# Performance work log

Hardware: AMD Instinct MI355X
Metric: run time of the kernel (lower is better)

Reference implementation:

```python
import jax, jax.numpy as jnp
import numpy as np

WH, WW = 8, 8
NUM_HEADS = 8
DIM = 256
MLP_HIDDEN = 1024
EPS = 1e-5


def _rel_pos_index(wh, ww):
    ch, cw = np.meshgrid(np.arange(wh), np.arange(ww), indexing='ij')
    flat = np.stack([ch.ravel(), cw.ravel()])            # (2, N)
    rel = flat[:, :, None] - flat[:, None, :]            # (2, N, N)
    rel = rel.transpose(1, 2, 0).copy()                  # (N, N, 2)
    rel[:, :, 0] += wh - 1
    rel[:, :, 1] += ww - 1
    rel[:, :, 0] *= 2 * ww - 1
    return jnp.asarray(rel.sum(-1))                      # (N, N) int

REL_IDX = _rel_pos_index(WH, WW)


def _layernorm(x, g, b):
    mu = x.mean(-1, keepdims=True)
    var = ((x - mu) ** 2).mean(-1, keepdims=True)
    return (x - mu) * jax.lax.rsqrt(var + EPS) * g + b


def _window_partition(x):
    B, H, W, C = x.shape
    x = x.reshape(B, H // WH, WH, W // WW, WW, C)
    return x.transpose(0, 1, 3, 2, 4, 5).reshape(-1, WH * WW, C)


def _window_reverse(w, B, H, W):
    C = w.shape[-1]
    x = w.reshape(B, H // WH, W // WW, WH, WW, C)
    return x.transpose(0, 1, 3, 2, 4, 5).reshape(B, H, W, C)


def _window_attn(qx, kvx, qw, qb, kvw, kvb, bias_table, pw, pb):
    # qx/kvx: [Bw, N, C]; weights stored as [in, out] (torch Linear transposed)
    Bw, N, C = qx.shape
    hd = C // NUM_HEADS
    scale = hd ** -0.5
    q = (qx @ qw + qb).reshape(Bw, N, NUM_HEADS, hd).transpose(0, 2, 1, 3) * scale
    kv = (kvx @ kvw + kvb).reshape(Bw, N, 2, NUM_HEADS, hd)
    k = kv[:, :, 0].transpose(0, 2, 1, 3)
    v = kv[:, :, 1].transpose(0, 2, 1, 3)
    attn = jnp.einsum('bhnd,bhmd->bhnm', q, k)
    bias = bias_table[REL_IDX.reshape(-1)].reshape(N, N, NUM_HEADS).transpose(2, 0, 1)
    attn = jax.nn.softmax(attn + bias[None], axis=-1)
    out = jnp.einsum('bhnm,bhmd->bhnd', attn, v).transpose(0, 2, 1, 3).reshape(Bw, N, C)
    return out @ pw + pb


def setup_inputs() -> dict:
    key = jax.random.key(0)
    ks = jax.random.split(key, 16)
    B, H, W, C = 4, 160, 160, DIM
    nW = (H // WH) * (W // WW)
    N = WH * WW
    n_bias = (2 * WH - 1) * (2 * WW - 1)  # 225
    s = 0.02
    return {
        'x': jax.random.normal(ks[0], (B, H, W, C), jnp.float32),
        'enc_feat': jax.random.normal(ks[1], (B, H, W, C), jnp.float32),
        'mask_matrix': jnp.zeros((nW, N, N), jnp.float32),
        'norm1_g': jnp.ones((C,), jnp.float32),
        'norm1_b': jnp.zeros((C,), jnp.float32),
        'q1_w': jax.random.normal(ks[2], (C, C), jnp.float32) * s,
        'q1_b': jnp.zeros((C,), jnp.float32),
        'kv1_w': jax.random.normal(ks[3], (C, 2 * C), jnp.float32) * s,
        'kv1_b': jnp.zeros((2 * C,), jnp.float32),
        'bias1': jax.random.normal(ks[4], (n_bias, NUM_HEADS), jnp.float32) * s,
        'proj1_w': jax.random.normal(ks[5], (C, C), jnp.float32) * s,
        'proj1_b': jnp.zeros((C,), jnp.float32),
        'q2_w': jax.random.normal(ks[6], (C, C), jnp.float32) * s,
        'q2_b': jnp.zeros((C,), jnp.float32),
        'kv2_w': jax.random.normal(ks[7], (C, 2 * C), jnp.float32) * s,
        'kv2_b': jnp.zeros((2 * C,), jnp.float32),
        'bias2': jax.random.normal(ks[8], (n_bias, NUM_HEADS), jnp.float32) * s,
        'proj2_w': jax.random.normal(ks[9], (C, C), jnp.float32) * s,
        'proj2_b': jnp.zeros((C,), jnp.float32),
        'norm2_g': jnp.ones((C,), jnp.float32),
        'norm2_b': jnp.zeros((C,), jnp.float32),
        'fc1_w': jax.random.normal(ks[10], (C, MLP_HIDDEN), jnp.float32) * s,
        'fc1_b': jnp.zeros((MLP_HIDDEN,), jnp.float32),
        'fc2_w': jax.random.normal(ks[11], (MLP_HIDDEN, C), jnp.float32) * s,
        'fc2_b': jnp.zeros((C,), jnp.float32),
    }


def reference(x, enc_feat, mask_matrix, norm1_g, norm1_b, q1_w, q1_b, kv1_w, kv1_b,
              bias1, proj1_w, proj1_b, q2_w, q2_b, kv2_w, kv2_b, bias2, proj2_w,
              proj2_b, norm2_g, norm2_b, fc1_w, fc1_b, fc2_w, fc2_b):
    # NOTE: the source forward never passes mask_matrix into attention; faithful here.
    B, H, W, C = x.shape
    shortcut = x
    xn = _layernorm(x, norm1_g, norm1_b)
    xw = _window_partition(xn)              # [B*nW, N, C]
    ew = _window_partition(enc_feat)        # [B*nW, N, C]
    # windowed self-attention with relative position bias
    xw = _window_attn(xw, xw, q1_w, q1_b, kv1_w, kv1_b, bias1, proj1_w, proj1_b)
    # windowed cross-attention to encoder features
    xw = _window_attn(xw, ew, q2_w, q2_b, kv2_w, kv2_b, bias2, proj2_w, proj2_b)
    x = shortcut + _window_reverse(xw, B, H, W)
    h = _layernorm(x, norm2_g, norm2_b)
    h = jax.nn.gelu(h @ fc1_w + fc1_b, approximate=False) @ fc2_w + fc2_b
    return x + h
```

## Files before the change

kernel.cpp:

```cpp
#include <hip/hip_runtime.h>

typedef __attribute__((ext_vector_type(4))) float f32x4;
typedef __attribute__((ext_vector_type(8))) short bf16x8;
typedef __attribute__((ext_vector_type(8))) unsigned short ushort8;
typedef unsigned short u16;
typedef unsigned int u32;

#define LDS_AS(p) ((__attribute__((address_space(3))) void*)(p))
#define GLB_AS(p) ((const __attribute__((address_space(1))) void*)(p))

__device__ __forceinline__ u16 f2b(float f) {
    u32 u = __builtin_bit_cast(u32, f);
    u32 r = (u + 0x7fffu + ((u >> 16) & 1u)) >> 16;
    return (u16)r;
}

struct PrepAll {
    const float* src[8];
    u16* dst[8];
    int K[8];
    int N[8];
};

__global__ __launch_bounds__(256) void prep_w(PrepAll p) {
    const int wi = blockIdx.y;
    const int K = p.K[wi], N = p.N[wi];
    const int e = blockIdx.x * 256 + threadIdx.x;
    if (e >= K * N) return;
    const int k = e / N, n = e % N;
    p.dst[wi][n * K + k] = f2b(p.src[wi][e]);
}

__global__ __launch_bounds__(64) void prep_bias(const float* __restrict__ t1,
                                                const float* __restrict__ t2,
                                                float* __restrict__ Bm) {
    const int j = threadIdx.x;
    const int i = blockIdx.x;
    const int hh = blockIdx.y;
    const int s = hh >> 3, h = hh & 7;
    const int idx = ((i >> 3) - (j >> 3) + 7) * 15 + ((i & 7) - (j & 7) + 7);
    const float* tab = s ? t2 : t1;
    Bm[(long)hh * 4096 + i * 64 + j] = tab[idx * 8 + h];
}

__global__ __launch_bounds__(256) void cast_bf(const float* __restrict__ in,
                                               u16* __restrict__ out) {
    const long i = (long)blockIdx.x * 256 + threadIdx.x;
    const float4 a = *(const float4*)(in + i * 8);
    const float4 b = *(const float4*)(in + i * 8 + 4);
    ushort8 o;
    o[0] = f2b(a.x); o[1] = f2b(a.y); o[2] = f2b(a.z); o[3] = f2b(a.w);
    o[4] = f2b(b.x); o[5] = f2b(b.y); o[6] = f2b(b.z); o[7] = f2b(b.w);
    *(ushort8*)(out + i * 8) = o;
}

__global__ __launch_bounds__(256) void ln256(const float* __restrict__ x,
                                             const float* __restrict__ g,
                                             const float* __restrict__ b,
                                             u16* __restrict__ out) {
    const int lane = threadIdx.x & 63;
    const long row = (long)blockIdx.x * 4 + (threadIdx.x >> 6);
    const float4 v = *(const float4*)(x + row * 256 + lane * 4);
    float s = v.x + v.y + v.z + v.w;
    float s2 = v.x * v.x + v.y * v.y + v.z * v.z + v.w * v.w;
#pragma unroll
    for (int off = 32; off > 0; off >>= 1) {
        s += __shfl_xor(s, off);
        s2 += __shfl_xor(s2, off);
    }
    const float mu = s * (1.f / 256.f);
    const float var = s2 * (1.f / 256.f) - mu * mu;
    const float rr = rsqrtf(var + 1e-5f);
    const int c = lane * 4;
    const float4 gv = *(const float4*)(g + c);
    const float4 bv = *(const float4*)(b + c);
    ushort4 o;
    o.x = f2b((v.x - mu) * rr * gv.x + bv.x);
    o.y = f2b((v.y - mu) * rr * gv.y + bv.y);
    o.z = f2b((v.z - mu) * rr * gv.z + bv.z);
    o.w = f2b((v.w - mu) * rr * gv.w + bv.w);
    *(ushort4*)(out + row * 256 + c) = o;
}

template <int EPI>
__global__ __launch_bounds__(256) void gemm128(const u16* __restrict__ A,
                                               const u16* __restrict__ Bt,
                                               const float* __restrict__ bias,
                                               const float* __restrict__ res,
                                               float scale, u16* outb, float* outf,
                                               int N, int K) {
    __shared__ u16 Alds[128 * 32];
    __shared__ u16 Blds[128 * 32];
    const int t = threadIdx.x;
    const int lane = t & 63;
    const int wave = t >> 6;
    const int wr = wave >> 1, wc = wave & 1;
    const int l15 = lane & 15, lg = lane >> 4;
    const long m0 = (long)blockIdx.x * 128;
    const int n0 = blockIdx.y * 128;

    const u16* Ag = A + (m0 + (t >> 2)) * K + (t & 3) * 8;
    const u16* Bg = Bt + (long)(n0 + (t >> 2)) * K + (t & 3) * 8;
    u16* Al = Alds + t * 8;
    u16* Bl = Blds + t * 8;

    f32x4 acc[4][4];
#pragma unroll
    for (int i = 0; i < 4; i++)
#pragma unroll
        for (int j = 0; j < 4; j++) acc[i][j] = (f32x4){0.f, 0.f, 0.f, 0.f};

    for (int k0 = 0; k0 < K; k0 += 32) {
        __syncthreads();
        __builtin_amdgcn_global_load_lds(GLB_AS(Ag + k0), LDS_AS(Al), 16, 0, 0);
        __builtin_amdgcn_global_load_lds(GLB_AS(Ag + (long)64 * K + k0), LDS_AS(Al + 2048), 16, 0, 0);
        __builtin_amdgcn_global_load_lds(GLB_AS(Bg + k0), LDS_AS(Bl), 16, 0, 0);
        __builtin_amdgcn_global_load_lds(GLB_AS(Bg + (long)64 * K + k0), LDS_AS(Bl + 2048), 16, 0, 0);
        __syncthreads();
        bf16x8 af[4], bfr[4];
#pragma unroll
        for (int i = 0; i < 4; i++)
            af[i] = *(const bf16x8*)(Alds + (wr * 64 + i * 16 + l15) * 32 + lg * 8);
#pragma unroll
        for (int i = 0; i < 4; i++)
            bfr[i] = *(const bf16x8*)(Blds + (wc * 64 + i * 16 + l15) * 32 + lg * 8);
#pragma unroll
        for (int mi = 0; mi < 4; mi++)
#pragma unroll
            for (int ni = 0; ni < 4; ni++)
                acc[mi][ni] = __builtin_amdgcn_mfma_f32_16x16x32_bf16(af[mi], bfr[ni], acc[mi][ni], 0, 0, 0);
    }

#pragma unroll
    for (int mi = 0; mi < 4; mi++) {
#pragma unroll
        for (int ni = 0; ni < 4; ni++) {
            const int col = n0 + wc * 64 + ni * 16 + l15;
            const float bv = bias[col];
#pragma unroll
            for (int r = 0; r < 4; r++) {
                const long row = m0 + wr * 64 + mi * 16 + lg * 4 + r;
                float v = acc[mi][ni][r] + bv;
                if (EPI == 1) v *= scale;
                if (EPI == 2) v = 0.5f * v * (1.f + erff(v * 0.70710678118f));
                const long idx = row * N + col;
                if (EPI == 3)
                    outf[idx] = v + res[idx];
                else
                    outb[idx] = f2b(v);
            }
        }
    }
}

__global__ __launch_bounds__(256) void attn64(const u16* __restrict__ Q,
                                              const u16* __restrict__ KV,
                                              const float* __restrict__ Bm,
                                              u16* __restrict__ AO) {
    __shared__ u16 Plds[4][64 * 72];
    __shared__ u16 Vt[4][32 * 72];
    const int lane = threadIdx.x & 63, wave = threadIdx.x >> 6;
    const int wh = blockIdx.x * 4 + wave;
    const int w = wh >> 3, h = wh & 7;
    const int b = w / 400, rem = w % 400;
    const int wy = rem / 20, wx = rem % 20;
    const long base_t = (long)b * 25600 + wy * 8 * 160 + wx * 8;
    const int l15 = lane & 15, lg = lane >> 4;

    bf16x8 qf[4], kf[4];
#pragma unroll
    for (int ti = 0; ti < 4; ti++) {
        const int r = ti * 16 + l15;
        const long tt = base_t + (r >> 3) * 160 + (r & 7);
        qf[ti] = *(const bf16x8*)(Q + tt * 256 + h * 32 + lg * 8);
        kf[ti] = *(const bf16x8*)(KV + tt * 512 + h * 32 + lg * 8);
    }
    const f32x4 zz = (f32x4){0.f, 0.f, 0.f, 0.f};
    f32x4 s[4][4];
#pragma unroll
    for (int ti = 0; ti < 4; ti++)
#pragma unroll
        for (int tj = 0; tj < 4; tj++)
            s[ti][tj] = __builtin_amdgcn_mfma_f32_16x16x32_bf16(qf[ti], kf[tj], zz, 0, 0, 0);

    {
        const long tt = base_t + (lane >> 3) * 160 + (lane & 7);
        const u16* vrow = KV + tt * 512 + 256 + h * 32;
#pragma unroll
        for (int cg = 0; cg < 4; cg++) {
            bf16x8 v8 = *(const bf16x8*)(vrow + cg * 8);
#pragma unroll
            for (int j = 0; j < 8; j++) Vt[wave][(cg * 8 + j) * 72 + lane] = (u16)v8[j];
        }
    }

    const float* Bh = Bm + h * 4096;
#pragma unroll
    for (int ti = 0; ti < 4; ti++) {
#pragma unroll
        for (int r = 0; r < 4; r++) {
            const int i = ti * 16 + lg * 4 + r;
            float vv[4];
            float m = -1e30f;
#pragma unroll
            for (int tj = 0; tj < 4; tj++) {
                vv[tj] = s[ti][tj][r] + Bh[i * 64 + tj * 16 + l15];
                m = fmaxf(m, vv[tj]);
            }
#pragma unroll
            for (int off = 1; off < 16; off <<= 1) m = fmaxf(m, __shfl_xor(m, off));
            float sum = 0.f;
#pragma unroll
            for (int tj = 0; tj < 4; tj++) {
                vv[tj] = __expf(vv[tj] - m);
                sum += vv[tj];
            }
#pragma unroll
            for (int off = 1; off < 16; off <<= 1) sum += __shfl_xor(sum, off);
            const float inv = 1.f / sum;
#pragma unroll
            for (int tj = 0; tj < 4; tj++)
                Plds[wave][i * 72 + tj * 16 + l15] = f2b(vv[tj] * inv);
        }
    }

    f32x4 o[4][2];
#pragma unroll
    for (int mi = 0; mi < 4; mi++)
#pragma unroll
        for (int n = 0; n < 2; n++) o[mi][n] = zz;
#pragma unroll
    for (int c = 0; c < 2; c++) {
        bf16x8 vf[2];
#pragma unroll
        for (int n = 0; n < 2; n++)
            vf[n] = *(const bf16x8*)(&Vt[wave][(n * 16 + l15) * 72 + c * 32 + lg * 8]);
#pragma unroll
        for (int mi = 0; mi < 4; mi++) {
            bf16x8 pf = *(const bf16x8*)(&Plds[wave][(mi * 16 + l15) * 72 + c * 32 + lg * 8]);
#pragma unroll
            for (int n = 0; n < 2; n++)
                o[mi][n] = __builtin_amdgcn_mfma_f32_16x16x32_bf16(pf, vf[n], o[mi][n], 0, 0, 0);
        }
    }
#pragma unroll
    for (int mi = 0; mi < 4; mi++) {
#pragma unroll
        for (int n = 0; n < 2; n++) {
#pragma unroll
            for (int r = 0; r < 4; r++) {
                const int i = mi * 16 + lg * 4 + r;
                const long tt = base_t + (i >> 3) * 160 + (i & 7);
                AO[tt * 256 + h * 32 + n * 16 + l15] = f2b(o[mi][n][r]);
            }
        }
    }
}

extern "C" void kernel_launch(void* const* d_in, const int* in_sizes, int n_in,
                              void* d_out, int out_size, void* d_ws, size_t ws_size,
                              hipStream_t stream) {
    const float* x    = (const float*)d_in[0];
    const float* enc  = (const float*)d_in[1];
    const float* n1g  = (const float*)d_in[3];
    const float* n1b  = (const float*)d_in[4];
    const float* q1w  = (const float*)d_in[5];
    const float* q1b  = (const float*)d_in[6];
    const float* kv1w = (const float*)d_in[7];
    const float* kv1b = (const float*)d_in[8];
    const float* bias1 = (const float*)d_in[9];
    const float* p1w  = (const float*)d_in[10];
    const float* p1b  = (const float*)d_in[11];
    const float* q2w  = (const float*)d_in[12];
    const float* q2b  = (const float*)d_in[13];
    const float* kv2w = (const float*)d_in[14];
    const float* kv2b = (const float*)d_in[15];
    const float* bias2 = (const float*)d_in[16];
    const float* p2w  = (const float*)d_in[17];
    const float* p2b  = (const float*)d_in[18];
    const float* n2g  = (const float*)d_in[19];
    const float* n2b  = (const float*)d_in[20];
    const float* f1w  = (const float*)d_in[21];
    const float* f1b  = (const float*)d_in[22];
    const float* f2w  = (const float*)d_in[23];
    const float* f2bias = (const float*)d_in[24];
    float* out = (float*)d_out;

    char* ws = (char*)d_ws;
    size_t off = 0;
    auto alloc = [&](size_t bytes) {
        char* p = ws + off;
        off += (bytes + 255) & ~(size_t)255;
        return p;
    };
    u16* Wt   = (u16*)alloc(1048576 * 2);
    float* Bm = (float*)alloc(16 * 4096 * 4);
    u16* xn   = (u16*)alloc(52428800);
    u16* qb   = (u16*)alloc(52428800);
    u16* kvb  = (u16*)alloc(104857600);
    u16* ao   = (u16*)alloc(52428800);
    u16* encb = (u16*)alloc(52428800);
    u16* h1   = (u16*)alloc(52428800);

    u16 *q1t = Wt, *kv1t = Wt + 65536, *p1t = Wt + 196608, *q2t = Wt + 262144,
        *kv2t = Wt + 327680, *p2t = Wt + 458752, *f1t = Wt + 524288, *f2t = Wt + 786432;

    PrepAll pa;
    pa.src[0] = q1w;  pa.dst[0] = q1t;  pa.K[0] = 256;  pa.N[0] = 256;
    pa.src[1] = kv1w; pa.dst[1] = kv1t; pa.K[1] = 256;  pa.N[1] = 512;
    pa.src[2] = p1w;  pa.dst[2] = p1t;  pa.K[2] = 256;  pa.N[2] = 256;
    pa.src[3] = q2w;  pa.dst[3] = q2t;  pa.K[3] = 256;  pa.N[3] = 256;
    pa.src[4] = kv2w; pa.dst[4] = kv2t; pa.K[4] = 256;  pa.N[4] = 512;
    pa.src[5] = p2w;  pa.dst[5] = p2t;  pa.K[5] = 256;  pa.N[5] = 256;
    pa.src[6] = f1w;  pa.dst[6] = f1t;  pa.K[6] = 256;  pa.N[6] = 1024;
    pa.src[7] = f2w;  pa.dst[7] = f2t;  pa.K[7] = 1024; pa.N[7] = 256;
    prep_w<<<dim3(1024, 8), 256, 0, stream>>>(pa);
    prep_bias<<<dim3(64, 16), 64, 0, stream>>>(bias1, bias2, Bm);
    cast_bf<<<dim3(12800), 256, 0, stream>>>(enc, encb);
    ln256<<<dim3(25600), 256, 0, stream>>>(x, n1g, n1b, xn);

    const float qscale = 0.17677669529663687f;

    gemm128<1><<<dim3(800, 2), 256, 0, stream>>>(xn, q1t, q1b, nullptr, qscale, qb, nullptr, 256, 256);
    gemm128<0><<<dim3(800, 4), 256, 0, stream>>>(xn, kv1t, kv1b, nullptr, 1.f, kvb, nullptr, 512, 256);
    attn64<<<dim3(3200), 256, 0, stream>>>(qb, kvb, Bm, ao);
    gemm128<0><<<dim3(800, 2), 256, 0, stream>>>(ao, p1t, p1b, nullptr, 1.f, xn, nullptr, 256, 256);

    gemm128<1><<<dim3(800, 2), 256, 0, stream>>>(xn, q2t, q2b, nullptr, qscale, qb, nullptr, 256, 256);
    gemm128<0><<<dim3(800, 4), 256, 0, stream>>>(encb, kv2t, kv2b, nullptr, 1.f, kvb, nullptr, 512, 256);
    attn64<<<dim3(3200), 256, 0, stream>>>(qb, kvb, Bm + 8 * 4096, ao);

    gemm128<3><<<dim3(800, 2), 256, 0, stream>>>(ao, p2t, p2b, x, 1.f, (u16*)nullptr, out, 256, 256);

    ln256<<<dim3(25600), 256, 0, stream>>>(out, n2g, n2b, qb);
    for (int c = 0; c < 4; c++) {
        const u16* xh = qb + (size_t)c * 25600 * 256;
        float* oc = out + (size_t)c * 25600 * 256;
        gemm128<2><<<dim3(200, 8), 256, 0, stream>>>(xh, f1t, f1b, nullptr, 1.f, h1, nullptr, 1024, 256);
        gemm128<3><<<dim3(200, 2), 256, 0, stream>>>(h1, f2t, f2bias, oc, 1.f, (u16*)nullptr, oc, 256, 1024);
    }
}
```

Measured before the change: 934.4 us.

## Double-buffer GEMM loads, fuse QKV projection, fold q-scale into weights, remap blocks

The GEMM kernel now double-buffers its LDS tiles, so global-to-LDS loads for step k+2 are issued while step k computes, with explicit waitcnt and barriers in place of the old two-syncthreads loop. Blocks are launched on a 1D grid remapped across groups of 8 for better cache locality. The first self-attention Q and KV projections are merged into one N=768 GEMM whose output attention reads with a stride parameter. The query scale is folded into the weights and biases during prep, which removes the scaled epilogue. The MLP now runs in 2 chunks instead of 4, reusing the KV buffer for the hidden activations, which saves memory but makes the buffer lifetimes more delicate.

```diff
diff --git a/kernel.cpp b/kernel.cpp
--- a/kernel.cpp
+++ b/kernel.cpp
@@ -20,6 +20,7 @@
     u16* dst[8];
     int K[8];
     int N[8];
+    float S[8];
 };
 
 __global__ __launch_bounds__(256) void prep_w(PrepAll p) {
@@ -28,7 +29,7 @@
     const int e = blockIdx.x * 256 + threadIdx.x;
     if (e >= K * N) return;
     const int k = e / N, n = e % N;
-    p.dst[wi][n * K + k] = f2b(p.src[wi][e]);
+    p.dst[wi][n * K + k] = f2b(p.src[wi][e] * p.S[wi]);
 }
 
 __global__ __launch_bounds__(64) void prep_bias(const float* __restrict__ t1,
@@ -41,6 +42,20 @@
     const int idx = ((i >> 3) - (j >> 3) + 7) * 15 + ((i & 7) - (j & 7) + 7);
     const float* tab = s ? t2 : t1;
     Bm[(long)hh * 4096 + i * 64 + j] = tab[idx * 8 + h];
+}
+
+__global__ __launch_bounds__(256) void prep_bcat(const float* __restrict__ q1b,
+                                                 const float* __restrict__ kv1b,
+                                                 const float* __restrict__ q2b,
+                                                 float qs, float* __restrict__ b1cat,
+                                                 float* __restrict__ q2bs) {
+    const int g = blockIdx.x * 256 + threadIdx.x;
+    if (g < 256) {
+        b1cat[g] = qs * q1b[g];
+        q2bs[g] = qs * q2b[g];
+    } else if (g < 768) {
+        b1cat[g] = kv1b[g - 256];
+    }
 }
 
 __global__ __launch_bounds__(256) void cast_bf(const float* __restrict__ in,
@@ -87,43 +102,65 @@
                                                const u16* __restrict__ Bt,
                                                const float* __restrict__ bias,
                                                const float* __restrict__ res,
-                                               float scale, u16* outb, float* outf,
-                                               int N, int K) {
-    __shared__ u16 Alds[128 * 32];
-    __shared__ u16 Blds[128 * 32];
+                                               u16* outb, float* outf,
+                                               int N, int K, int Nt) {
+    __shared__ u16 lds[2][2][128 * 32];
     const int t = threadIdx.x;
     const int lane = t & 63;
     const int wave = t >> 6;
     const int wr = wave >> 1, wc = wave & 1;
     const int l15 = lane & 15, lg = lane >> 4;
-    const long m0 = (long)blockIdx.x * 128;
-    const int n0 = blockIdx.y * 128;
+
+    const int per = gridDim.x >> 3;
+    const int id2 = (blockIdx.x & 7) * per + (blockIdx.x >> 3);
+    const int bm = id2 / Nt, bn = id2 % Nt;
+    const long m0 = (long)bm * 128;
+    const int n0 = bn * 128;
 
     const u16* Ag = A + (m0 + (t >> 2)) * K + (t & 3) * 8;
     const u16* Bg = Bt + (long)(n0 + (t >> 2)) * K + (t & 3) * 8;
-    u16* Al = Alds + t * 8;
-    u16* Bl = Blds + t * 8;
-
-    f32x4 acc[4][4];
-#pragma unroll
-    for (int i = 0; i < 4; i++)
-#pragma unroll
-        for (int j = 0; j < 4; j++) acc[i][j] = (f32x4){0.f, 0.f, 0.f, 0.f};
-
-    for (int k0 = 0; k0 < K; k0 += 32) {
-        __syncthreads();
+
+    const int nt = K >> 5;
+
+    auto stage = [&](int b, int k0) {
+        u16* Al = lds[b][0] + t * 8;
+        u16* Bl = lds[b][1] + t * 8;
         __builtin_amdgcn_global_load_lds(GLB_AS(Ag + k0), LDS_AS(Al), 16, 0, 0);
         __builtin_amdgcn_global_load_lds(GLB_AS(Ag + (long)64 * K + k0), LDS_AS(Al + 2048), 16, 0, 0);
         __builtin_amdgcn_global_load_lds(GLB_AS(Bg + k0), LDS_AS(Bl), 16, 0, 0);
         __builtin_amdgcn_global_load_lds(GLB_AS(Bg + (long)64 * K + k0), LDS_AS(Bl + 2048), 16, 0, 0);
-        __syncthreads();
+    };
+
+    f32x4 acc[4][4];
+#pragma unroll
+    for (int i = 0; i < 4; i++)
+#pragma unroll
+        for (int j = 0; j < 4; j++) acc[i][j] = (f32x4){0.f, 0.f, 0.f, 0.f};
+
+    stage(0, 0);
+    if (nt > 1) stage(1, 32);
+
+    for (int tt = 0; tt < nt; ++tt) {
+        const int cur = tt & 1;
+        if (tt < nt - 1)
+            asm volatile("s_waitcnt vmcnt(4)" ::: "memory");
+        else
+            asm volatile("s_waitcnt vmcnt(0)" ::: "memory");
+        __builtin_amdgcn_s_barrier();
+
         bf16x8 af[4], bfr[4];
 #pragma unroll
         for (int i = 0; i < 4; i++)
-            af[i] = *(const bf16x8*)(Alds + (wr * 64 + i * 16 + l15) * 32 + lg * 8);
+            af[i] = *(const bf16x8*)(lds[cur][0] + (wr * 64 + i * 16 + l15) * 32 + lg * 8);
 #pragma unroll
         for (int i = 0; i < 4; i++)
-            bfr[i] = *(const bf16x8*)(Blds + (wc * 64 + i * 16 + l15) * 32 + lg * 8);
+            bfr[i] = *(const bf16x8*)(lds[cur][1] + (wc * 64 + i * 16 + l15) * 32 + lg * 8);
+        asm volatile("s_waitcnt lgkmcnt(0)" ::: "memory");
+        __builtin_amdgcn_sched_barrier(0);
+        __builtin_amdgcn_s_barrier();
+
+        if (tt + 2 < nt) stage(cur, (tt + 2) * 32);
+
 #pragma unroll
         for (int mi = 0; mi < 4; mi++)
 #pragma unroll
@@ -141,7 +178,6 @@
             for (int r = 0; r < 4; r++) {
                 const long row = m0 + wr * 64 + mi * 16 + lg * 4 + r;
                 float v = acc[mi][ni][r] + bv;
-                if (EPI == 1) v *= scale;
                 if (EPI == 2) v = 0.5f * v * (1.f + erff(v * 0.70710678118f));
                 const long idx = row * N + col;
                 if (EPI == 3)
@@ -153,8 +189,8 @@
     }
 }
 
-__global__ __launch_bounds__(256) void attn64(const u16* __restrict__ Q,
-                                              const u16* __restrict__ KV,
+__global__ __launch_bounds__(256) void attn64(const u16* __restrict__ Q, int qs,
+                                              const u16* __restrict__ KV, int ks,
                                               const float* __restrict__ Bm,
                                               u16* __restrict__ AO) {
     __shared__ u16 Plds[4][64 * 72];
@@ -172,8 +208,8 @@
     for (int ti = 0; ti < 4; ti++) {
         const int r = ti * 16 + l15;
         const long tt = base_t + (r >> 3) * 160 + (r & 7);
-        qf[ti] = *(const bf16x8*)(Q + tt * 256 + h * 32 + lg * 8);
-        kf[ti] = *(const bf16x8*)(KV + tt * 512 + h * 32 + lg * 8);
+        qf[ti] = *(const bf16x8*)(Q + tt * qs + h * 32 + lg * 8);
+        kf[ti] = *(const bf16x8*)(KV + tt * ks + h * 32 + lg * 8);
     }
     const f32x4 zz = (f32x4){0.f, 0.f, 0.f, 0.f};
     f32x4 s[4][4];
@@ -185,7 +221,7 @@
 
     {
         const long tt = base_t + (lane >> 3) * 160 + (lane & 7);
-        const u16* vrow = KV + tt * 512 + 256 + h * 32;
+        const u16* vrow = KV + tt * ks + 256 + h * 32;
 #pragma unroll
         for (int cg = 0; cg < 4; cg++) {
             bf16x8 v8 = *(const bf16x8*)(vrow + cg * 8);
@@ -293,50 +329,54 @@
         off += (bytes + 255) & ~(size_t)255;
         return p;
     };
-    u16* Wt   = (u16*)alloc(1048576 * 2);
-    float* Bm = (float*)alloc(16 * 4096 * 4);
-    u16* xn   = (u16*)alloc(52428800);
-    u16* qb   = (u16*)alloc(52428800);
-    u16* kvb  = (u16*)alloc(104857600);
-    u16* ao   = (u16*)alloc(52428800);
-    u16* encb = (u16*)alloc(52428800);
-    u16* h1   = (u16*)alloc(52428800);
-
-    u16 *q1t = Wt, *kv1t = Wt + 65536, *p1t = Wt + 196608, *q2t = Wt + 262144,
+    u16* Wt    = (u16*)alloc(1048576 * 2);
+    float* Bm  = (float*)alloc(16 * 4096 * 4);
+    float* b1c = (float*)alloc(768 * 4);
+    float* q2s = (float*)alloc(256 * 4);
+    u16* xn    = (u16*)alloc(52428800);
+    u16* qb    = (u16*)alloc(52428800);
+    u16* kvb   = (u16*)alloc(104857600);
+    u16* ao    = (u16*)alloc(52428800);
+    u16* encb  = (u16*)alloc(52428800);
+
+    u16* qkv = qb;
+    u16* h1  = kvb;
+
+    u16 *q1t = Wt, *p1t = Wt + 196608, *q2t = Wt + 262144,
         *kv2t = Wt + 327680, *p2t = Wt + 458752, *f1t = Wt + 524288, *f2t = Wt + 786432;
 
+    const float qscale = 0.17677669529663687f;
+
     PrepAll pa;
-    pa.src[0] = q1w;  pa.dst[0] = q1t;  pa.K[0] = 256;  pa.N[0] = 256;
-    pa.src[1] = kv1w; pa.dst[1] = kv1t; pa.K[1] = 256;  pa.N[1] = 512;
-    pa.src[2] = p1w;  pa.dst[2] = p1t;  pa.K[2] = 256;  pa.N[2] = 256;
-    pa.src[3] = q2w;  pa.dst[3] = q2t;  pa.K[3] = 256;  pa.N[3] = 256;
-    pa.src[4] = kv2w; pa.dst[4] = kv2t; pa.K[4] = 256;  pa.N[4] = 512;
-    pa.src[5] = p2w;  pa.dst[5] = p2t;  pa.K[5] = 256;  pa.N[5] = 256;
-    pa.src[6] = f1w;  pa.dst[6] = f1t;  pa.K[6] = 256;  pa.N[6] = 1024;
-    pa.src[7] = f2w;  pa.dst[7] = f2t;  pa.K[7] = 1024; pa.N[7] = 256;
+    pa.src[0] = q1w;  pa.dst[0] = q1t;          pa.K[0] = 256;  pa.N[0] = 256;  pa.S[0] = qscale;
+    pa.src[1] = kv1w; pa.dst[1] = Wt + 65536;   pa.K[1] = 256;  pa.N[1] = 512;  pa.S[1] = 1.f;
+    pa.src[2] = p1w;  pa.dst[2] = p1t;          pa.K[2] = 256;  pa.N[2] = 256;  pa.S[2] = 1.f;
+    pa.src[3] = q2w;  pa.dst[3] = q2t;          pa.K[3] = 256;  pa.N[3] = 256;  pa.S[3] = qscale;
+    pa.src[4] = kv2w; pa.dst[4] = kv2t;         pa.K[4] = 256;  pa.N[4] = 512;  pa.S[4] = 1.f;
+    pa.src[5] = p2w;  pa.dst[5] = p2t;          pa.K[5] = 256;  pa.N[5] = 256;  pa.S[5] = 1.f;
+    pa.src[6] = f1w;  pa.dst[6] = f1t;          pa.K[6] = 256;  pa.N[6] = 1024; pa.S[6] = 1.f;
+    pa.src[7] = f2w;  pa.dst[7] = f2t;          pa.K[7] = 1024; pa.N[7] = 256;  pa.S[7] = 1.f;
     prep_w<<<dim3(1024, 8), 256, 0, stream>>>(pa);
     prep_bias<<<dim3(64, 16), 64, 0, stream>>>(bias1, bias2, Bm);
+    prep_bcat<<<dim3(3), 256, 0, stream>>>(q1b, kv1b, q2b, qscale, b1c, q2s);
     cast_bf<<<dim3(12800), 256, 0, stream>>>(enc, encb);
     ln256<<<dim3(25600), 256, 0, stream>>>(x, n1g, n1b, xn);
 
-    const float qscale = 0.17677669529663687f;
-
-    gemm128<1><<<dim3(800, 2), 256, 0, stream>>>(xn, q1t, q1b, nullptr, qscale, qb, nullptr, 256, 256);
-    gemm128<0><<<dim3(800, 4), 256, 0, stream>>>(xn, kv1t, kv1b, nullptr, 1.f, kvb, nullptr, 512, 256);
-    attn64<<<dim3(3200), 256, 0, stream>>>(qb, kvb, Bm, ao);
-    gemm128<0><<<dim3(800, 2), 256, 0, stream>>>(ao, p1t, p1b, nullptr, 1.f, xn, nullptr, 256, 256);
-
-    gemm128<1><<<dim3(800, 2), 256, 0, stream>>>(xn, q2t, q2b, nullptr, qscale, qb, nullptr, 256, 256);
-    gemm128<0><<<dim3(800, 4), 256, 0, stream>>>(encb, kv2t, kv2b, nullptr, 1.f, kvb, nullptr, 512, 256);
-    attn64<<<dim3(3200), 256, 0, stream>>>(qb, kvb, Bm + 8 * 4096, ao);
-
-    gemm128<3><<<dim3(800, 2), 256, 0, stream>>>(ao, p2t, p2b, x, 1.f, (u16*)nullptr, out, 256, 256);
+    gemm128<0><<<dim3(4800), 256, 0, stream>>>(xn, q1t, b1c, nullptr, qkv, nullptr, 768, 256, 6);
+    attn64<<<dim3(3200), 256, 0, stream>>>(qkv, 768, qkv + 256, 768, Bm, ao);
+    gemm128<0><<<dim3(1600), 256, 0, stream>>>(ao, p1t, p1b, nullptr, xn, nullptr, 256, 256, 2);
+
+    gemm128<0><<<dim3(1600), 256, 0, stream>>>(xn, q2t, q2s, nullptr, qb, nullptr, 256, 256, 2);
+    gemm128<0><<<dim3(3200), 256, 0, stream>>>(encb, kv2t, kv2b, nullptr, kvb, nullptr, 512, 256, 4);
+    attn64<<<dim3(3200), 256, 0, stream>>>(qb, 256, kvb, 512, Bm + 8 * 4096, ao);
+
+    gemm128<3><<<dim3(1600), 256, 0, stream>>>(ao, p2t, p2b, x, (u16*)nullptr, out, 256, 256, 2);
 
     ln256<<<dim3(25600), 256, 0, stream>>>(out, n2g, n2b, qb);
-    for (int c = 0; c < 4; c++) {
-        const u16* xh = qb + (size_t)c * 25600 * 256;
-        float* oc = out + (size_t)c * 25600 * 256;
-        gemm128<2><<<dim3(200, 8), 256, 0, stream>>>(xh, f1t, f1b, nullptr, 1.f, h1, nullptr, 1024, 256);
-        gemm128<3><<<dim3(200, 2), 256, 0, stream>>>(h1, f2t, f2bias, oc, 1.f, (u16*)nullptr, oc, 256, 1024);
-    }
-}
+    for (int c = 0; c < 2; c++) {
+        const u16* xh = qb + (size_t)c * 51200 * 256;
+        float* oc = out + (size_t)c * 51200 * 256;
+        gemm128<2><<<dim3(3200), 256, 0, stream>>>(xh, f1t, f1b, nullptr, h1, nullptr, 1024, 256, 8);
+        gemm128<3><<<dim3(800), 256, 0, stream>>>(h1, f2t, f2bias, oc, (u16*)nullptr, oc, 256, 1024, 2);
+    }
+}
```

New measurement: 800.9 us. 14.3% less time.
